# Performance work log

Measured on AMD Instinct MI355X. Metric: run time of the kernel, lower is better.

The kernel has to match this reference:

```python
import jax, jax.numpy as jnp
import numpy as np

D_MODEL = 1024
NUM_HEADS = 16
D_K = D_MODEL // NUM_HEADS


def setup_inputs() -> dict:
    key = jax.random.key(0)
    k1, k2, k3, kq, kk, kv, ko = jax.random.split(key, 7)
    B, S = 4, 2048
    scale = 1.0 / np.sqrt(D_MODEL)
    return {
        "Q_in": jax.random.normal(k1, (B, S, D_MODEL), dtype=jnp.float32),
        "K_in": jax.random.normal(k2, (B, S, D_MODEL), dtype=jnp.float32),
        "V_in": jax.random.normal(k3, (B, S, D_MODEL), dtype=jnp.float32),
        "W_q": jax.random.normal(kq, (D_MODEL, D_MODEL), dtype=jnp.float32) * scale,
        "W_k": jax.random.normal(kk, (D_MODEL, D_MODEL), dtype=jnp.float32) * scale,
        "W_v": jax.random.normal(kv, (D_MODEL, D_MODEL), dtype=jnp.float32) * scale,
        "W_o": jax.random.normal(ko, (D_MODEL, D_MODEL), dtype=jnp.float32) * scale,
    }


def _split_heads(x):
    B, S, _ = x.shape
    return x.reshape(B, S, NUM_HEADS, D_K).transpose(0, 2, 1, 3)  # [B,H,S,d_k]


def reference(Q_in, K_in, V_in, W_q, W_k, W_v, W_o):
    # nn.Linear: y = x @ W.T ; here W_* stored as [out, in] equivalent square,
    # use x @ W.T convention to match torch.
    Q = _split_heads(Q_in @ W_q.T)
    K = _split_heads(K_in @ W_k.T)
    V = _split_heads(V_in @ W_v.T)
    scores = jnp.einsum("bhqd,bhkd->bhqk", Q, K) / jnp.sqrt(jnp.float32(D_K))
    attn = jax.nn.softmax(scores, axis=-1)  # [B,H,S,S]
    out = jnp.einsum("bhqk,bhkd->bhqd", attn, V)
    B, H, S, dk = out.shape
    concat = out.transpose(0, 2, 1, 3).reshape(B, S, H * dk)
    return concat @ W_o.T
```

## Files before the change

### kernel.cpp

```cpp
#include <hip/hip_runtime.h>
#include <math.h>

typedef __bf16 bf16x8v __attribute__((ext_vector_type(8)));
typedef short bf16x4s __attribute__((ext_vector_type(4)));
typedef float f32x4 __attribute__((ext_vector_type(4)));

__device__ __forceinline__ void async_copy16(void* lds, const void* g) {
  __builtin_amdgcn_global_load_lds(
      (const __attribute__((address_space(1))) void*)g,
      (__attribute__((address_space(3))) void*)lds, 16, 0, 0);
}

struct CastArgs {
  const float* s[7];
  __bf16* d[7];
};
__global__ __launch_bounds__(256) void cast_kernel(CastArgs a) {
  const int t = blockIdx.y;
  const int n = (t < 3) ? 8388608 : 1048576;
  const int i = (blockIdx.x * 256 + threadIdx.x) * 8;
  if (i >= n) return;
  const float4 v0 = *(const float4*)(a.s[t] + i);
  const float4 v1 = *(const float4*)(a.s[t] + i + 4);
  bf16x8v o;
  o[0] = (__bf16)v0.x; o[1] = (__bf16)v0.y; o[2] = (__bf16)v0.z; o[3] = (__bf16)v0.w;
  o[4] = (__bf16)v1.x; o[5] = (__bf16)v1.y; o[6] = (__bf16)v1.z; o[7] = (__bf16)v1.w;
  *(bf16x8v*)(a.d[t] + i) = o;
}

template <int MODE, typename OutT>
__global__ __launch_bounds__(256) void gemm_bt(const __bf16* A, const __bf16* B,
                                               OutT* C,
                                               const __bf16* A2, const __bf16* B2,
                                               OutT* C2,
                                               int M, int N, int K) {
  __shared__ __bf16 As[128 * 64];
  __shared__ __bf16 Bs[128 * 64];
  if (blockIdx.z == 1) { A = A2; B = B2; C = C2; }
  const int tid = threadIdx.x;
  const int wave = tid >> 6, lane = tid & 63;
  const int lgrp = lane >> 4, lmod = lane & 15;
  const int bm = (MODE == 3 ? blockIdx.y : blockIdx.x) * 128;
  const int bn = (MODE == 3 ? blockIdx.x : blockIdx.y) * 128;
  const int wm = (wave >> 1) * 64, wn = (wave & 1) * 64;

  f32x4 acc[4][4];
#pragma unroll
  for (int mi = 0; mi < 4; mi++)
#pragma unroll
    for (int ni = 0; ni < 4; ni++)
#pragma unroll
      for (int r = 0; r < 4; r++) acc[mi][ni][r] = 0.f;

  for (int kt = 0; kt < K; kt += 64) {
#pragma unroll
    for (int i = 0; i < 4; i++) {
      const int s = i * 256 + tid;
      const int r = s >> 3, cb = s & 7;
      const int gc = (cb ^ (r & 7)) * 8;
      async_copy16(&As[s * 8], &A[(size_t)(bm + r) * K + kt + gc]);
      async_copy16(&Bs[s * 8], &B[(size_t)(bn + r) * K + kt + gc]);
    }
    __syncthreads();
#pragma unroll
    for (int ks = 0; ks < 2; ks++) {
      bf16x8v af[4], bf[4];
#pragma unroll
      for (int mi = 0; mi < 4; mi++) {
        const int row = wm + mi * 16 + lmod;
        af[mi] = *(const bf16x8v*)&As[row * 64 + ((ks * 4 + lgrp) ^ (row & 7)) * 8];
      }
#pragma unroll
      for (int ni = 0; ni < 4; ni++) {
        const int row = wn + ni * 16 + lmod;
        bf[ni] = *(const bf16x8v*)&Bs[row * 64 + ((ks * 4 + lgrp) ^ (row & 7)) * 8];
      }
#pragma unroll
      for (int mi = 0; mi < 4; mi++)
#pragma unroll
        for (int ni = 0; ni < 4; ni++)
          acc[mi][ni] = __builtin_amdgcn_mfma_f32_16x16x32_bf16(af[mi], bf[ni],
                                                                acc[mi][ni], 0, 0, 0);
    }
    __syncthreads();
  }

#pragma unroll
  for (int mi = 0; mi < 4; mi++)
#pragma unroll
    for (int ni = 0; ni < 4; ni++)
#pragma unroll
      for (int r = 0; r < 4; r++) {
        const int row = bm + wm + mi * 16 + lgrp * 4 + r;
        const int col = bn + wn + ni * 16 + lmod;
        if (MODE == 0) {
          C[(size_t)row * N + col] = (OutT)acc[mi][ni][r];
        } else if (MODE == 1) {
          C[(size_t)(row >> 11) * 2097152 + (size_t)(col >> 6) * 131072 +
            (size_t)(row & 2047) * 64 + (col & 63)] = (OutT)acc[mi][ni][r];
        } else {
          C[(size_t)(col >> 11) * 2097152 + (size_t)(row >> 6) * 131072 +
            (size_t)(row & 63) * 2048 + (col & 2047)] = (OutT)acc[mi][ni][r];
        }
      }
}

__global__ __launch_bounds__(256) void attn_kernel(const __bf16* __restrict__ Qh,
                                                   const __bf16* __restrict__ Kh,
                                                   const __bf16* __restrict__ Vt,
                                                   __bf16* __restrict__ O) {
  __shared__ __bf16 Ks[128 * 64];
  __shared__ __bf16 Vts[64 * 128];

  const int tid = threadIdx.x;
  const int wave = tid >> 6, lane = tid & 63;
  const int lgrp = lane >> 4, lmod = lane & 15;
  const int qt = blockIdx.y, y = blockIdx.x;
  const size_t hb = (size_t)y * 131072;
  const __bf16* Qb = Qh + hb + (size_t)qt * 128 * 64;
  const __bf16* Kb = Kh + hb;
  const __bf16* Vb = Vt + hb;
  const int wq0 = wave * 32;

  const float qscale = 0.125f * 1.44269504f;
  bf16x8v qf[2][2];
#pragma unroll
  for (int qi = 0; qi < 2; qi++)
#pragma unroll
    for (int ks = 0; ks < 2; ks++) {
      bf16x8v q = *(const bf16x8v*)&Qb[(wq0 + qi * 16 + lmod) * 64 + ks * 32 + lgrp * 8];
#pragma unroll
      for (int j = 0; j < 8; j++) q[j] = (__bf16)((float)q[j] * qscale);
      qf[qi][ks] = q;
    }

  float m_run[2] = {-INFINITY, -INFINITY};
  float l_run[2] = {0.f, 0.f};
  f32x4 oacc[2][4];
#pragma unroll
  for (int qi = 0; qi < 2; qi++)
#pragma unroll
    for (int nd = 0; nd < 4; nd++)
#pragma unroll
      for (int r = 0; r < 4; r++) oacc[qi][nd][r] = 0.f;

  for (int kv0 = 0; kv0 < 2048; kv0 += 128) {
#pragma unroll
    for (int i = 0; i < 4; i++) {
      const int s = i * 256 + tid;
      {
        const int r = s >> 3, cb = s & 7;
        async_copy16(&Ks[s * 8], &Kb[(size_t)(kv0 + r) * 64 + (cb ^ (r & 7)) * 8]);
      }
      {
        const int r = s >> 4, cb = s & 15;
        async_copy16(&Vts[s * 8], &Vb[(size_t)r * 2048 + kv0 + (cb ^ (r & 7)) * 8]);
      }
    }
    __syncthreads();

#pragma unroll 1
    for (int half = 0; half < 2; half++) {
      f32x4 st[4][2];
#pragma unroll
      for (int t = 0; t < 4; t++)
#pragma unroll
        for (int qi = 0; qi < 2; qi++)
#pragma unroll
          for (int r = 0; r < 4; r++) st[t][qi][r] = 0.f;
#pragma unroll
      for (int ks = 0; ks < 2; ks++) {
#pragma unroll
        for (int t = 0; t < 4; t++) {
          const int row = half * 64 + t * 16 + lmod;
          const bf16x8v kf =
              *(const bf16x8v*)&Ks[row * 64 + ((ks * 4 + lgrp) ^ (row & 7)) * 8];
#pragma unroll
          for (int qi = 0; qi < 2; qi++)
            st[t][qi] = __builtin_amdgcn_mfma_f32_16x16x32_bf16(kf, qf[qi][ks],
                                                                st[t][qi], 0, 0, 0);
        }
      }

      float alpha_l[2], mnew_l[2];
#pragma unroll
      for (int qi = 0; qi < 2; qi++) {
        float rmax = st[0][qi][0];
#pragma unroll
        for (int t = 0; t < 4; t++)
#pragma unroll
          for (int r = 0; r < 4; r++) rmax = fmaxf(rmax, st[t][qi][r]);
        rmax = fmaxf(rmax, __shfl_xor(rmax, 16));
        rmax = fmaxf(rmax, __shfl_xor(rmax, 32));
        const float mnew = fmaxf(m_run[qi], rmax);
        alpha_l[qi] = __builtin_amdgcn_exp2f(m_run[qi] - mnew);
        mnew_l[qi] = mnew;
        m_run[qi] = mnew;
      }
#pragma unroll
      for (int qi = 0; qi < 2; qi++)
#pragma unroll
        for (int r = 0; r < 4; r++) {
          const float ar = __shfl(alpha_l[qi], lgrp * 4 + r);
#pragma unroll
          for (int nd = 0; nd < 4; nd++) oacc[qi][nd][r] *= ar;
        }

      float psum[2] = {0.f, 0.f};
#pragma unroll
      for (int t = 0; t < 4; t++) {
        bf16x4s vf[4];
        const int kvb = half * 64 + t * 16 + lgrp * 4;
#pragma unroll
        for (int nd = 0; nd < 4; nd++) {
          const int row = nd * 16 + lmod;
          vf[nd] =
              *(const bf16x4s*)&Vts[row * 128 + ((kvb >> 3) ^ (row & 7)) * 8 + (kvb & 7)];
        }
#pragma unroll
        for (int qi = 0; qi < 2; qi++) {
          union { __bf16 b[4]; bf16x4s s; } pf;
#pragma unroll
          for (int r = 0; r < 4; r++) {
            const float p = __builtin_amdgcn_exp2f(st[t][qi][r] - mnew_l[qi]);
            psum[qi] += p;
            pf.b[r] = (__bf16)p;
          }
#pragma unroll
          for (int nd = 0; nd < 4; nd++)
            oacc[qi][nd] = __builtin_amdgcn_mfma_f32_16x16x16bf16_1k(pf.s, vf[nd],
                                                                     oacc[qi][nd], 0, 0, 0);
        }
      }
#pragma unroll
      for (int qi = 0; qi < 2; qi++) {
        float ps = psum[qi];
        ps += __shfl_xor(ps, 16);
        ps += __shfl_xor(ps, 32);
        l_run[qi] = l_run[qi] * alpha_l[qi] + ps;
      }
    }
    __syncthreads();
  }

  const int b = y >> 4, h = y & 15;
#pragma unroll
  for (int qi = 0; qi < 2; qi++) {
    const float linv = 1.f / l_run[qi];
#pragma unroll
    for (int r = 0; r < 4; r++) {
      const float inv = __shfl(linv, lgrp * 4 + r);
      const int srow = qt * 128 + wq0 + qi * 16 + lgrp * 4 + r;
      const size_t base = ((size_t)(b * 2048 + srow)) * 1024 + h * 64;
#pragma unroll
      for (int nd = 0; nd < 4; nd++)
        O[base + nd * 16 + lmod] = (__bf16)(oacc[qi][nd][r] * inv);
    }
  }
}

extern "C" void kernel_launch(void* const* d_in, const int* in_sizes, int n_in,
                              void* d_out, int out_size, void* d_ws, size_t ws_size,
                              hipStream_t stream) {
  const float* Qin = (const float*)d_in[0];
  const float* Kin = (const float*)d_in[1];
  const float* Vin = (const float*)d_in[2];
  const float* Wq = (const float*)d_in[3];
  const float* Wk = (const float*)d_in[4];
  const float* Wv = (const float*)d_in[5];
  const float* Wo = (const float*)d_in[6];
  float* out = (float*)d_out;

  __bf16* base = (__bf16*)d_ws;
  __bf16* Qbf = base;
  __bf16* Kbf = base + 8388608;
  __bf16* Vbf = base + 16777216;
  __bf16* Wqb = base + 25165824;
  __bf16* Wkb = base + 26214400;
  __bf16* Wvb = base + 27262976;
  __bf16* Wob = base + 28311552;
  __bf16* Qh = base + 29360128;
  __bf16* Kh = base + 37748736;
  __bf16* Vt = base + 46137344;
  __bf16* AO = Qbf;

  CastArgs ca;
  ca.s[0] = Qin; ca.s[1] = Kin; ca.s[2] = Vin;
  ca.s[3] = Wq;  ca.s[4] = Wk;  ca.s[5] = Wv;  ca.s[6] = Wo;
  ca.d[0] = Qbf; ca.d[1] = Kbf; ca.d[2] = Vbf;
  ca.d[3] = Wqb; ca.d[4] = Wkb; ca.d[5] = Wvb; ca.d[6] = Wob;
  cast_kernel<<<dim3(4096, 7), 256, 0, stream>>>(ca);

  const int M = 8192, N = 1024, K = 1024;
  dim3 bb(256);
  gemm_bt<1, __bf16><<<dim3(64, 8, 2), bb, 0, stream>>>(Qbf, Wqb, Qh,
                                                        Kbf, Wkb, Kh, M, N, K);
  gemm_bt<3, __bf16><<<dim3(64, 8), bb, 0, stream>>>(Wvb, Vbf, Vt,
                                                     nullptr, nullptr, nullptr,
                                                     1024, 8192, K);
  attn_kernel<<<dim3(64, 16), bb, 0, stream>>>(Qh, Kh, Vt, AO);
  gemm_bt<0, float><<<dim3(64, 8), bb, 0, stream>>>(AO, Wob, out,
                                                    nullptr, nullptr, nullptr,
                                                    M, N, K);
}
```

Measured before the change: 393.3 us.

## Skip online-softmax rescale when max grows little; defer row-sum reduction; prioritize MFMA

Adds a lazy rescaling threshold to the flash-attention inner loop. The running max and the output rescale are updated only when some row's new max exceeds the old one by more than 8 (log2 domain), which the wave decides with a wave-wide vote. The per-lane partial row sums are now kept unreduced until the epilogue, which removes cross-lane shuffles from every tile. The max reduction becomes a tree, and s_setprio raises wave priority around the MFMA blocks to help interleave waves. The cost is a branch and probabilities up to 2^8 before normalization, which could affect bf16 precision.

```diff
diff --git a/kernel.cpp b/kernel.cpp
--- a/kernel.cpp
+++ b/kernel.cpp
@@ -175,36 +175,46 @@
           const int row = half * 64 + t * 16 + lmod;
           const bf16x8v kf =
               *(const bf16x8v*)&Ks[row * 64 + ((ks * 4 + lgrp) ^ (row & 7)) * 8];
+          __builtin_amdgcn_s_setprio(1);
 #pragma unroll
           for (int qi = 0; qi < 2; qi++)
             st[t][qi] = __builtin_amdgcn_mfma_f32_16x16x32_bf16(kf, qf[qi][ks],
                                                                 st[t][qi], 0, 0, 0);
-        }
-      }
-
-      float alpha_l[2], mnew_l[2];
+          __builtin_amdgcn_s_setprio(0);
+        }
+      }
+
+      float rmax_l[2];
 #pragma unroll
       for (int qi = 0; qi < 2; qi++) {
-        float rmax = st[0][qi][0];
+        float tm[4];
 #pragma unroll
         for (int t = 0; t < 4; t++)
-#pragma unroll
-          for (int r = 0; r < 4; r++) rmax = fmaxf(rmax, st[t][qi][r]);
+          tm[t] = fmaxf(fmaxf(st[t][qi][0], st[t][qi][1]),
+                        fmaxf(st[t][qi][2], st[t][qi][3]));
+        float rmax = fmaxf(fmaxf(tm[0], tm[1]), fmaxf(tm[2], tm[3]));
         rmax = fmaxf(rmax, __shfl_xor(rmax, 16));
         rmax = fmaxf(rmax, __shfl_xor(rmax, 32));
-        const float mnew = fmaxf(m_run[qi], rmax);
-        alpha_l[qi] = __builtin_amdgcn_exp2f(m_run[qi] - mnew);
-        mnew_l[qi] = mnew;
-        m_run[qi] = mnew;
-      }
-#pragma unroll
-      for (int qi = 0; qi < 2; qi++)
-#pragma unroll
-        for (int r = 0; r < 4; r++) {
-          const float ar = __shfl(alpha_l[qi], lgrp * 4 + r);
-#pragma unroll
-          for (int nd = 0; nd < 4; nd++) oacc[qi][nd][r] *= ar;
-        }
+        rmax_l[qi] = rmax;
+      }
+      if (!__all(rmax_l[0] - m_run[0] <= 8.f && rmax_l[1] - m_run[1] <= 8.f)) {
+        float alpha_l[2];
+#pragma unroll
+        for (int qi = 0; qi < 2; qi++) {
+          const float mnew = fmaxf(m_run[qi], rmax_l[qi]);
+          alpha_l[qi] = __builtin_amdgcn_exp2f(m_run[qi] - mnew);
+          m_run[qi] = mnew;
+          l_run[qi] *= alpha_l[qi];
+        }
+#pragma unroll
+        for (int qi = 0; qi < 2; qi++)
+#pragma unroll
+          for (int r = 0; r < 4; r++) {
+            const float ar = __shfl(alpha_l[qi], lgrp * 4 + r);
+#pragma unroll
+            for (int nd = 0; nd < 4; nd++) oacc[qi][nd][r] *= ar;
+          }
+      }
 
       float psum[2] = {0.f, 0.f};
 #pragma unroll
@@ -222,23 +232,20 @@
           union { __bf16 b[4]; bf16x4s s; } pf;
 #pragma unroll
           for (int r = 0; r < 4; r++) {
-            const float p = __builtin_amdgcn_exp2f(st[t][qi][r] - mnew_l[qi]);
+            const float p = __builtin_amdgcn_exp2f(st[t][qi][r] - m_run[qi]);
             psum[qi] += p;
             pf.b[r] = (__bf16)p;
           }
+          __builtin_amdgcn_s_setprio(1);
 #pragma unroll
           for (int nd = 0; nd < 4; nd++)
             oacc[qi][nd] = __builtin_amdgcn_mfma_f32_16x16x16bf16_1k(pf.s, vf[nd],
                                                                      oacc[qi][nd], 0, 0, 0);
-        }
-      }
-#pragma unroll
-      for (int qi = 0; qi < 2; qi++) {
-        float ps = psum[qi];
-        ps += __shfl_xor(ps, 16);
-        ps += __shfl_xor(ps, 32);
-        l_run[qi] = l_run[qi] * alpha_l[qi] + ps;
-      }
+          __builtin_amdgcn_s_setprio(0);
+        }
+      }
+      l_run[0] += psum[0];
+      l_run[1] += psum[1];
     }
     __syncthreads();
   }
@@ -246,7 +253,10 @@
   const int b = y >> 4, h = y & 15;
 #pragma unroll
   for (int qi = 0; qi < 2; qi++) {
-    const float linv = 1.f / l_run[qi];
+    float l = l_run[qi];
+    l += __shfl_xor(l, 16);
+    l += __shfl_xor(l, 32);
+    const float linv = 1.f / l;
 #pragma unroll
     for (int r = 0; r < 4; r++) {
       const float inv = __shfl(linv, lgrp * 4 + r);
```

Measured after the change: 380.1 us. 3.4% less time.

## Switch attention to 32x32x16 MFMA tiles with lazy rescaling and permlane P packing

Applied to the files above, without the earlier changes.

Rewrites the attention inner loop to use 32x32x16 bf16 MFMAs for both QK^T and PV instead of 16x16 instructions. The P fragment is built in registers with packed bf16 conversion and permlane32 swaps, so it can feed the second MFMA directly. The running max is only updated, and the accumulators rescaled, when the new block max exceeds the old one by more than 8 in log2 space. MFMA issue priority is raised with s_setprio. The aim is fewer MFMA issues and less softmax/shuffle overhead per tile. The risks are the larger accumulator register footprint and possible fp32 growth of unnormalized values under lazy rescaling.

```diff
diff --git a/kernel.cpp b/kernel.cpp
--- a/kernel.cpp
+++ b/kernel.cpp
@@ -2,8 +2,8 @@
 #include <math.h>
 
 typedef __bf16 bf16x8v __attribute__((ext_vector_type(8)));
-typedef short bf16x4s __attribute__((ext_vector_type(4)));
 typedef float f32x4 __attribute__((ext_vector_type(4)));
+typedef float f32x16 __attribute__((ext_vector_type(16)));
 
 __device__ __forceinline__ void async_copy16(void* lds, const void* g) {
   __builtin_amdgcn_global_load_lds(
@@ -114,7 +114,7 @@
 
   const int tid = threadIdx.x;
   const int wave = tid >> 6, lane = tid & 63;
-  const int lgrp = lane >> 4, lmod = lane & 15;
+  const int l31 = lane & 31, hi = lane >> 5;
   const int qt = blockIdx.y, y = blockIdx.x;
   const size_t hb = (size_t)y * 131072;
   const __bf16* Qb = Qh + hb + (size_t)qt * 128 * 64;
@@ -123,26 +123,22 @@
   const int wq0 = wave * 32;
 
   const float qscale = 0.125f * 1.44269504f;
-  bf16x8v qf[2][2];
-#pragma unroll
-  for (int qi = 0; qi < 2; qi++)
-#pragma unroll
-    for (int ks = 0; ks < 2; ks++) {
-      bf16x8v q = *(const bf16x8v*)&Qb[(wq0 + qi * 16 + lmod) * 64 + ks * 32 + lgrp * 8];
-#pragma unroll
-      for (int j = 0; j < 8; j++) q[j] = (__bf16)((float)q[j] * qscale);
-      qf[qi][ks] = q;
-    }
-
-  float m_run[2] = {-INFINITY, -INFINITY};
-  float l_run[2] = {0.f, 0.f};
-  f32x4 oacc[2][4];
-#pragma unroll
-  for (int qi = 0; qi < 2; qi++)
-#pragma unroll
-    for (int nd = 0; nd < 4; nd++)
-#pragma unroll
-      for (int r = 0; r < 4; r++) oacc[qi][nd][r] = 0.f;
+  bf16x8v qf[4];
+#pragma unroll
+  for (int ks = 0; ks < 4; ks++) {
+    bf16x8v q = *(const bf16x8v*)&Qb[(wq0 + l31) * 64 + ks * 16 + hi * 8];
+#pragma unroll
+    for (int j = 0; j < 8; j++) q[j] = (__bf16)((float)q[j] * qscale);
+    qf[ks] = q;
+  }
+
+  float m_run = -INFINITY;
+  float l_run = 0.f;
+  f32x16 oacc[2];
+#pragma unroll
+  for (int nd = 0; nd < 2; nd++)
+#pragma unroll
+    for (int r = 0; r < 16; r++) oacc[nd][r] = 0.f;
 
   for (int kv0 = 0; kv0 < 2048; kv0 += 128) {
 #pragma unroll
@@ -161,101 +157,95 @@
 
 #pragma unroll 1
     for (int half = 0; half < 2; half++) {
-      f32x4 st[4][2];
-#pragma unroll
-      for (int t = 0; t < 4; t++)
-#pragma unroll
-        for (int qi = 0; qi < 2; qi++)
-#pragma unroll
-          for (int r = 0; r < 4; r++) st[t][qi][r] = 0.f;
-#pragma unroll
-      for (int ks = 0; ks < 2; ks++) {
-#pragma unroll
-        for (int t = 0; t < 4; t++) {
-          const int row = half * 64 + t * 16 + lmod;
-          const bf16x8v kf =
-              *(const bf16x8v*)&Ks[row * 64 + ((ks * 4 + lgrp) ^ (row & 7)) * 8];
-#pragma unroll
-          for (int qi = 0; qi < 2; qi++)
-            st[t][qi] = __builtin_amdgcn_mfma_f32_16x16x32_bf16(kf, qf[qi][ks],
-                                                                st[t][qi], 0, 0, 0);
+      f32x16 st[2];
+#pragma unroll
+      for (int kvt = 0; kvt < 2; kvt++)
+#pragma unroll
+        for (int r = 0; r < 16; r++) st[kvt][r] = 0.f;
+#pragma unroll
+      for (int ks = 0; ks < 4; ks++) {
+        const int sl = ((ks * 2 + hi) ^ (l31 & 7)) * 8;
+        const bf16x8v kf0 =
+            *(const bf16x8v*)&Ks[(half * 64 + l31) * 64 + sl];
+        const bf16x8v kf1 =
+            *(const bf16x8v*)&Ks[(half * 64 + 32 + l31) * 64 + sl];
+        __builtin_amdgcn_s_setprio(1);
+        st[0] = __builtin_amdgcn_mfma_f32_32x32x16_bf16(kf0, qf[ks], st[0], 0, 0, 0);
+        st[1] = __builtin_amdgcn_mfma_f32_32x32x16_bf16(kf1, qf[ks], st[1], 0, 0, 0);
+        __builtin_amdgcn_s_setprio(0);
+      }
+
+      float b[16];
+#pragma unroll
+      for (int j = 0; j < 16; j++) b[j] = fmaxf(st[0][j], st[1][j]);
+#pragma unroll
+      for (int s = 8; s > 0; s >>= 1)
+#pragma unroll
+        for (int j = 0; j < 8; j++)
+          if (j < s) b[j] = fmaxf(b[j], b[j + s]);
+      float rmax = b[0];
+      rmax = fmaxf(rmax, __shfl_xor(rmax, 32));
+
+      if (!__all(rmax - m_run <= 8.f)) {
+        const float mnew = fmaxf(m_run, rmax);
+        const float alpha = __builtin_amdgcn_exp2f(m_run - mnew);
+        m_run = mnew;
+        l_run *= alpha;
+#pragma unroll
+        for (int r = 0; r < 16; r++) {
+          const float ar = __shfl(alpha, (r & 3) + 8 * (r >> 2) + 4 * hi);
+          oacc[0][r] *= ar;
+          oacc[1][r] *= ar;
         }
       }
 
-      float alpha_l[2], mnew_l[2];
-#pragma unroll
-      for (int qi = 0; qi < 2; qi++) {
-        float rmax = st[0][qi][0];
-#pragma unroll
-        for (int t = 0; t < 4; t++)
-#pragma unroll
-          for (int r = 0; r < 4; r++) rmax = fmaxf(rmax, st[t][qi][r]);
-        rmax = fmaxf(rmax, __shfl_xor(rmax, 16));
-        rmax = fmaxf(rmax, __shfl_xor(rmax, 32));
-        const float mnew = fmaxf(m_run[qi], rmax);
-        alpha_l[qi] = __builtin_amdgcn_exp2f(m_run[qi] - mnew);
-        mnew_l[qi] = mnew;
-        m_run[qi] = mnew;
-      }
-#pragma unroll
-      for (int qi = 0; qi < 2; qi++)
-#pragma unroll
-        for (int r = 0; r < 4; r++) {
-          const float ar = __shfl(alpha_l[qi], lgrp * 4 + r);
-#pragma unroll
-          for (int nd = 0; nd < 4; nd++) oacc[qi][nd][r] *= ar;
+      float psum = 0.f;
+#pragma unroll
+      for (int kvt = 0; kvt < 2; kvt++) {
+#pragma unroll
+        for (int sub = 0; sub < 2; sub++) {
+          const int ks2 = kvt * 2 + sub;
+          const int vs = ((half * 8 + ks2 * 2 + hi) ^ (l31 & 7)) * 8;
+          const bf16x8v vf0 = *(const bf16x8v*)&Vts[l31 * 128 + vs];
+          const bf16x8v vf1 = *(const bf16x8v*)&Vts[(32 + l31) * 128 + vs];
+          const int o = sub * 8;
+          float p[8];
+#pragma unroll
+          for (int j = 0; j < 8; j++) {
+            p[j] = __builtin_amdgcn_exp2f(st[kvt][o + j] - m_run);
+            psum += p[j];
+          }
+          unsigned x0, y0, x1, y1;
+          asm("v_cvt_pk_bf16_f32 %0, %1, %2" : "=v"(x0) : "v"(p[0]), "v"(p[1]));
+          asm("v_cvt_pk_bf16_f32 %0, %1, %2" : "=v"(y0) : "v"(p[4]), "v"(p[5]));
+          asm("v_cvt_pk_bf16_f32 %0, %1, %2" : "=v"(x1) : "v"(p[2]), "v"(p[3]));
+          asm("v_cvt_pk_bf16_f32 %0, %1, %2" : "=v"(y1) : "v"(p[6]), "v"(p[7]));
+          asm("v_permlane32_swap_b32 %0, %1" : "+v"(x0), "+v"(y0));
+          asm("v_permlane32_swap_b32 %0, %1" : "+v"(x1), "+v"(y1));
+          union { unsigned u[4]; bf16x8v v; } af;
+          af.u[0] = x0; af.u[1] = x1; af.u[2] = y0; af.u[3] = y1;
+          __builtin_amdgcn_s_setprio(1);
+          oacc[0] = __builtin_amdgcn_mfma_f32_32x32x16_bf16(af.v, vf0, oacc[0], 0, 0, 0);
+          oacc[1] = __builtin_amdgcn_mfma_f32_32x32x16_bf16(af.v, vf1, oacc[1], 0, 0, 0);
+          __builtin_amdgcn_s_setprio(0);
         }
-
-      float psum[2] = {0.f, 0.f};
-#pragma unroll
-      for (int t = 0; t < 4; t++) {
-        bf16x4s vf[4];
-        const int kvb = half * 64 + t * 16 + lgrp * 4;
-#pragma unroll
-        for (int nd = 0; nd < 4; nd++) {
-          const int row = nd * 16 + lmod;
-          vf[nd] =
-              *(const bf16x4s*)&Vts[row * 128 + ((kvb >> 3) ^ (row & 7)) * 8 + (kvb & 7)];
-        }
-#pragma unroll
-        for (int qi = 0; qi < 2; qi++) {
-          union { __bf16 b[4]; bf16x4s s; } pf;
-#pragma unroll
-          for (int r = 0; r < 4; r++) {
-            const float p = __builtin_amdgcn_exp2f(st[t][qi][r] - mnew_l[qi]);
-            psum[qi] += p;
-            pf.b[r] = (__bf16)p;
-          }
-#pragma unroll
-          for (int nd = 0; nd < 4; nd++)
-            oacc[qi][nd] = __builtin_amdgcn_mfma_f32_16x16x16bf16_1k(pf.s, vf[nd],
-                                                                     oacc[qi][nd], 0, 0, 0);
-        }
-      }
-#pragma unroll
-      for (int qi = 0; qi < 2; qi++) {
-        float ps = psum[qi];
-        ps += __shfl_xor(ps, 16);
-        ps += __shfl_xor(ps, 32);
-        l_run[qi] = l_run[qi] * alpha_l[qi] + ps;
-      }
-    }
-    __syncthreads();
-  }
-
+      }
+      l_run += psum;
+    }
+    __syncthreads();
+  }
+
+  l_run += __shfl_xor(l_run, 32);
+  const float linv = 1.f / l_run;
   const int b = y >> 4, h = y & 15;
 #pragma unroll
-  for (int qi = 0; qi < 2; qi++) {
-    const float linv = 1.f / l_run[qi];
-#pragma unroll
-    for (int r = 0; r < 4; r++) {
-      const float inv = __shfl(linv, lgrp * 4 + r);
-      const int srow = qt * 128 + wq0 + qi * 16 + lgrp * 4 + r;
-      const size_t base = ((size_t)(b * 2048 + srow)) * 1024 + h * 64;
-#pragma unroll
-      for (int nd = 0; nd < 4; nd++)
-        O[base + nd * 16 + lmod] = (__bf16)(oacc[qi][nd][r] * inv);
-    }
+  for (int r = 0; r < 16; r++) {
+    const int q = (r & 3) + 8 * (r >> 2) + 4 * hi;
+    const float inv = __shfl(linv, q);
+    const int srow = qt * 128 + wq0 + q;
+    const size_t base = ((size_t)(b * 2048 + srow)) * 1024 + h * 64;
+    O[base + l31] = (__bf16)(oacc[0][r] * inv);
+    O[base + 32 + l31] = (__bf16)(oacc[1][r] * inv);
   }
 }
 
```

New measurement: 376.6 us. 4.2% less time.
